# Optimization experiments

Hardware: AMD Instinct MI355X
Metric: run time of the kernel (lower is better)

Reference implementation:

```python
import jax, jax.numpy as jnp
import numpy as np

B, S, E = 8, 1024, 1024
H, HS = 16, 64  # num_heads, head_size; H*HS == E


def setup_inputs() -> dict:
    key = jax.random.key(0)
    ks = jax.random.split(key, 6)
    scale = 1.0 / np.sqrt(E)
    x = jax.random.normal(ks[0], (B, S, E), dtype=jnp.float32)
    # per-head projection weights stacked: [H, E, HS] (Linear(n_embd, head_size, bias=False))
    Wq = jax.random.normal(ks[1], (H, E, HS), dtype=jnp.float32) * scale
    Wk = jax.random.normal(ks[2], (H, E, HS), dtype=jnp.float32) * scale
    Wv = jax.random.normal(ks[3], (H, E, HS), dtype=jnp.float32) * scale
    # output projection Linear(n_embd, n_embd): torch weight [out, in] plus bias
    Wproj = jax.random.normal(ks[4], (E, E), dtype=jnp.float32) * scale
    bproj = jax.random.normal(ks[5], (E,), dtype=jnp.float32) * scale
    return {"x": x, "Wq": Wq, "Wk": Wk, "Wv": Wv, "Wproj": Wproj, "bproj": bproj}


def reference(x, Wq, Wk, Wv, Wproj, bproj):
    # q,k,v: [B, H, S, HS]
    q = jnp.einsum('bse,hed->bhsd', x, Wq)
    k = jnp.einsum('bse,hed->bhsd', x, Wk)
    v = jnp.einsum('bse,hed->bhsd', x, Wv)
    scores = jnp.einsum('bhsd,bhtd->bhst', q, k) * (HS ** -0.5)  # [B,H,S,S]
    causal = jnp.tril(jnp.ones((S, S), dtype=bool))
    scores = jnp.where(causal, scores, jnp.finfo(scores.dtype).min)
    attn = jax.nn.softmax(scores, axis=-1)
    out = jnp.einsum('bhst,bhtd->bhsd', attn, v)         # [B,H,S,HS]
    out = out.transpose(0, 2, 1, 3).reshape(B, S, H * HS)  # concat heads -> [B,S,E]
    return out @ Wproj.T + bproj  # dropout p=0 is identity
```

## Files before the change

kernel.cpp:

```cpp
#include <hip/hip_runtime.h>
#include <stdint.h>

#define DEVI __device__ __forceinline__

typedef __attribute__((ext_vector_type(8))) short bf16x8;
typedef __attribute__((ext_vector_type(4))) float floatx4;
typedef __attribute__((ext_vector_type(16))) float floatx16;

constexpr int Bb = 8, Ss = 1024, Ee = 1024, Hh = 16, HSs = 64;
constexpr int Mq = Bb * Ss;
constexpr int Nqkv = 3 * Hh * HSs;
constexpr int Kd = Ee;

DEVI unsigned short f2bf(float x) {
  union { float f; uint32_t u; } v; v.f = x;
  uint32_t r = v.u + 0x7FFFu + ((v.u >> 16) & 1u);
  return (unsigned short)(r >> 16);
}

DEVI uint32_t pk2(float a, float b) {
  return (uint32_t)f2bf(a) | ((uint32_t)f2bf(b) << 16);
}

DEVI bf16x8 mkfrag(uint32_t a, uint32_t b, uint32_t c, uint32_t d) {
  union { uint32_t u[4]; bf16x8 v; } x;
  x.u[0] = a; x.u[1] = b; x.u[2] = c; x.u[3] = d;
  return x.v;
}

DEVI floatx4 mfma16(bf16x8 a, bf16x8 b, floatx4 c) {
  return __builtin_amdgcn_mfma_f32_16x16x32_bf16(a, b, c, 0, 0, 0);
}
DEVI floatx16 mfma32(bf16x8 a, bf16x8 b, floatx16 c) {
  return __builtin_amdgcn_mfma_f32_32x32x16_bf16(a, b, c, 0, 0, 0);
}

DEVI void gload_lds16(const void* g, void* l) {
  __builtin_amdgcn_global_load_lds(
      (const __attribute__((address_space(1))) uint32_t*)(uintptr_t)g,
      (__attribute__((address_space(3))) uint32_t*)(uint32_t)(uintptr_t)l,
      16, 0, 0);
}

__global__ void cvt_f32_bf16(const float* __restrict__ in, unsigned short* __restrict__ out, int n) {
  int i = (blockIdx.x * blockDim.x + threadIdx.x) * 4;
  if (i >= n) return;
  float4 v = *(const float4*)&in[i];
  ushort4 o;
  o.x = f2bf(v.x); o.y = f2bf(v.y); o.z = f2bf(v.z); o.w = f2bf(v.w);
  *(ushort4*)(void*)&out[i] = o;
}

__global__ void cvt_wqkv(const float* __restrict__ Wq, const float* __restrict__ Wk,
                         const float* __restrict__ Wv, unsigned short* __restrict__ out) {
  __shared__ float tile[64][65];
  const int k0 = blockIdx.x * 64;
  const int hh = blockIdx.y;
  const int qkv = hh >> 4, h = hh & 15;
  const float* W = (qkv == 0) ? Wq : ((qkv == 1) ? Wk : Wv);
  const float scale = (qkv == 0) ? (0.125f * 1.44269504f) : 1.0f;
  const float* src = W + (size_t)h * Ee * HSs;
  const int c = threadIdx.x & 63, r4 = threadIdx.x >> 6;
#pragma unroll
  for (int rr = 0; rr < 16; ++rr) {
    int row = rr * 4 + r4;
    tile[row][c] = src[(size_t)(k0 + row) * HSs + c] * scale;
  }
  __syncthreads();
  const int base_n = qkv * 1024 + h * 64;
#pragma unroll
  for (int rr = 0; rr < 16; ++rr) {
    int hs = rr * 4 + r4;
    out[(size_t)(base_n + hs) * Kd + k0 + c] = f2bf(tile[c][hs]);
  }
}

__global__ __launch_bounds__(256, 4) void gemm_qkv_db32(
    const unsigned short* __restrict__ A, const unsigned short* __restrict__ Bt,
    unsigned short* __restrict__ Qb, unsigned short* __restrict__ Kb,
    unsigned short* __restrict__ Vtb, int Kdim) {
  __shared__ __align__(16) unsigned short As[2][128 * 32];
  __shared__ __align__(16) unsigned short Bs[2][128 * 32];
  const int tid = threadIdx.x;
  const int lane = tid & 63;
  const int wid = tid >> 6;
  const int wm = wid >> 1, wn = wid & 1;
  const int m0 = blockIdx.y * 128;
  const int n0 = blockIdx.x * 128;
  const int srow = lane >> 2;
  const int NT = Kdim >> 5;

  floatx4 acc[4][4];
#pragma unroll
  for (int i = 0; i < 4; ++i)
#pragma unroll
    for (int j = 0; j < 4; ++j) acc[i][j] = (floatx4)0.f;

  auto stage = [&](int kt, int b) {
#pragma unroll
    for (int i = 0; i < 2; ++i) {
      const int g = wid * 2 + i;
      const int row = g * 16 + srow;
      const int sch = (lane & 3) ^ ((row + (row >> 2)) & 3);
      gload_lds16(A + (size_t)(m0 + row) * Kdim + kt * 32 + sch * 8, &As[b][g * 512]);
      gload_lds16(Bt + (size_t)(n0 + row) * Kdim + kt * 32 + sch * 8, &Bs[b][g * 512]);
    }
  };

  stage(0, 0);
  __syncthreads();

  const int c = lane >> 4;
  for (int kt = 0; kt < NT; ++kt) {
    const int cur = kt & 1;
    if (kt + 1 < NT) stage(kt + 1, cur ^ 1);
    const unsigned short* Ap = As[cur];
    const unsigned short* Bp = Bs[cur];
    bf16x8 af[4], bf[4];
#pragma unroll
    for (int i = 0; i < 4; ++i) {
      const int ra = wm * 64 + i * 16 + (lane & 15);
      af[i] = *(const bf16x8*)&Ap[ra * 32 + ((c ^ ((ra + (ra >> 2)) & 3)) << 3)];
      const int rb = wn * 64 + i * 16 + (lane & 15);
      bf[i] = *(const bf16x8*)&Bp[rb * 32 + ((c ^ ((rb + (rb >> 2)) & 3)) << 3)];
    }
#pragma unroll
    for (int i = 0; i < 4; ++i)
#pragma unroll
      for (int j = 0; j < 4; ++j) acc[i][j] = mfma16(af[i], bf[j], acc[i][j]);
    __syncthreads();
  }

  const int mrow0 = m0 + wm * 64 + ((lane >> 4) << 2);
  const int ncol0 = n0 + wn * 64 + (lane & 15);
#pragma unroll
  for (int i = 0; i < 4; ++i) {
#pragma unroll
    for (int j = 0; j < 4; ++j) {
      const int n = ncol0 + j * 16;
      const int qkv = n >> 10;
      const int h = (n & 1023) >> 6;
      const int hs = n & 63;
#pragma unroll
      for (int r = 0; r < 4; ++r) {
        const int m = mrow0 + i * 16 + r;
        const int b = m >> 10, s = m & 1023;
        const unsigned short bv = f2bf(acc[i][j][r]);
        if (qkv == 0)
          Qb[(((size_t)b * Hh + h) * Ss + s) * HSs + hs] = bv;
        else if (qkv == 1)
          Kb[(((size_t)b * Hh + h) * Ss + s) * HSs + hs] = bv;
        else
          Vtb[(((size_t)b * Hh + h) * HSs + hs) * Ss + s] = bv;
      }
    }
  }
}

__global__ __launch_bounds__(256, 2) void gemm_proj(
    const unsigned short* __restrict__ A, const unsigned short* __restrict__ Bt,
    float* __restrict__ Out, const float* __restrict__ bias, int Ndim, int Kdim) {
  __shared__ __align__(16) unsigned short As[128 * 64];
  __shared__ __align__(16) unsigned short Bs[128 * 64];
  const int tid = threadIdx.x;
  const int lane = tid & 63;
  const int wid = tid >> 6;
  const int wm = wid >> 1, wn = wid & 1;
  const int m0 = blockIdx.y * 128;
  const int n0 = blockIdx.x * 128;

  floatx4 acc[4][4];
#pragma unroll
  for (int i = 0; i < 4; ++i)
#pragma unroll
    for (int j = 0; j < 4; ++j) acc[i][j] = (floatx4)0.f;

  const int srow = lane >> 3;
  const int schunk = (lane & 7) ^ srow;

  for (int kt = 0; kt < Kdim; kt += 64) {
#pragma unroll
    for (int j = 0; j < 4; ++j) {
      const int g = wid * 4 + j;
      const int row = g * 8 + srow;
      gload_lds16(A + (size_t)(m0 + row) * Kdim + kt + schunk * 8, &As[g * 8 * 64]);
      gload_lds16(Bt + (size_t)(n0 + row) * Kdim + kt + schunk * 8, &Bs[g * 8 * 64]);
    }
    __syncthreads();
#pragma unroll
    for (int kk = 0; kk < 2; ++kk) {
      const int c = kk * 4 + (lane >> 4);
      bf16x8 af[4], bf[4];
#pragma unroll
      for (int i = 0; i < 4; ++i) {
        const int ra = wm * 64 + i * 16 + (lane & 15);
        af[i] = *(const bf16x8*)&As[ra * 64 + ((c ^ (ra & 7)) << 3)];
        const int rb = wn * 64 + i * 16 + (lane & 15);
        bf[i] = *(const bf16x8*)&Bs[rb * 64 + ((c ^ (rb & 7)) << 3)];
      }
#pragma unroll
      for (int i = 0; i < 4; ++i)
#pragma unroll
        for (int j = 0; j < 4; ++j) acc[i][j] = mfma16(af[i], bf[j], acc[i][j]);
    }
    __syncthreads();
  }

  const int mrow0 = m0 + wm * 64 + ((lane >> 4) << 2);
  const int ncol0 = n0 + wn * 64 + (lane & 15);
#pragma unroll
  for (int j = 0; j < 4; ++j) {
    const int n = ncol0 + j * 16;
    const float bj = bias[n];
#pragma unroll
    for (int i = 0; i < 4; ++i) {
#pragma unroll
      for (int r = 0; r < 4; ++r) {
        const int m = mrow0 + i * 16 + r;
        Out[(size_t)m * Ndim + n] = acc[i][j][r] + bj;
      }
    }
  }
}

__global__ __launch_bounds__(512, 4) void attn(
    const unsigned short* __restrict__ Qb, const unsigned short* __restrict__ Kb,
    const unsigned short* __restrict__ Vtb, unsigned short* __restrict__ Ob) {
  __shared__ __align__(16) unsigned short Ks[3][64 * 64];
  __shared__ __align__(16) unsigned short Vs[3][64 * 64];

  const int tid = threadIdx.x;
  const int lane = tid & 63;
  const int wid = tid >> 6;
  const int ln = lane & 31;
  const int hi = lane >> 5;
  const int bh = blockIdx.x & 127;
  const int qs = blockIdx.x >> 7;
  const int q0 = (3 - qs) * 256;
  const int bI = bh >> 4, hI = bh & 15;
  const unsigned short* Qp = Qb + (size_t)bh * Ss * HSs;
  const unsigned short* Kp = Kb + (size_t)bh * Ss * HSs;
  const unsigned short* Vp = Vtb + (size_t)bh * HSs * Ss;
  const int qw = q0 + wid * 32;
  const int q = qw + ln;

  bf16x8 qf[4];
#pragma unroll
  for (int kc = 0; kc < 4; ++kc)
    qf[kc] = *(const bf16x8*)&Qp[(size_t)q * 64 + kc * 16 + hi * 8];

  floatx16 oacc[2];
  oacc[0] = (floatx16)0.f;
  oacc[1] = (floatx16)0.f;
  float mrow = -3.0e38f, lrow = 0.f;

  const int srow = lane >> 3;
  const int schunk = (lane & 7) ^ srow;
  const int nt = (q0 >> 6) + 4;

  auto stageKV = [&](int t, int b) {
    const int row = wid * 8 + srow;
    gload_lds16(Kp + (size_t)(t * 64 + row) * 64 + schunk * 8, &Ks[b][wid * 512]);
    gload_lds16(Vp + (size_t)row * Ss + t * 64 + schunk * 8, &Vs[b][wid * 512]);
  };

  stageKV(0, 0);
  stageKV(1, 1);
  asm volatile("s_waitcnt vmcnt(2)" ::: "memory");
  __builtin_amdgcn_s_barrier();

  for (int t = 0; t < nt; ++t) {
    const int cur = t % 3;
    const bool pf = (t + 2 < nt);
    if (pf) stageKV(t + 2, (t + 2) % 3);
    const int t0 = t * 64;

    if (t0 <= qw + 31) {
      const unsigned short* Kc = Ks[cur];
      const unsigned short* Vc = Vs[cur];
      floatx16 sc[2];
#pragma unroll
      for (int tt = 0; tt < 2; ++tt) {
        floatx16 s = (floatx16)0.f;
        __builtin_amdgcn_s_setprio(1);
#pragma unroll
        for (int kc = 0; kc < 4; ++kc) {
          const int row = tt * 32 + ln;
          bf16x8 kf = *(const bf16x8*)&Kc[row * 64 + ((((kc << 1) | hi) ^ (ln & 7)) << 3)];
          s = mfma32(kf, qf[kc], s);
        }
        __builtin_amdgcn_s_setprio(0);
        sc[tt] = s;
      }
      if (t0 + 63 > qw) {
#pragma unroll
        for (int tt = 0; tt < 2; ++tt)
#pragma unroll
          for (int r = 0; r < 16; ++r) {
            const int tg = t0 + tt * 32 + (r & 3) + 8 * (r >> 2) + 4 * hi;
            if (tg > q) sc[tt][r] = -1e30f;
          }
      }
      float mx = sc[0][0];
#pragma unroll
      for (int tt = 0; tt < 2; ++tt)
#pragma unroll
        for (int r = 0; r < 16; ++r) mx = fmaxf(mx, sc[tt][r]);
      mx = fmaxf(mx, __shfl_xor(mx, 32));
      const float mnew = fmaxf(mrow, mx);
      const float scal = __builtin_amdgcn_exp2f(mrow - mnew);
      mrow = mnew;
      float ss = 0.f;
#pragma unroll
      for (int tt = 0; tt < 2; ++tt)
#pragma unroll
        for (int r = 0; r < 16; ++r) {
          const float p = __builtin_amdgcn_exp2f(sc[tt][r] - mnew);
          sc[tt][r] = p;
          ss += p;
        }
      ss += __shfl_xor(ss, 32);
      lrow = lrow * scal + ss;
#pragma unroll
      for (int dt = 0; dt < 2; ++dt)
#pragma unroll
        for (int r = 0; r < 16; ++r) oacc[dt][r] *= scal;

      bf16x8 pf_[4];
#pragma unroll
      for (int tt = 0; tt < 2; ++tt)
#pragma unroll
        for (int fb = 0; fb < 2; ++fb) {
          const int b = fb * 8;
          const uint32_t w0 = pk2(sc[tt][b + 0], sc[tt][b + 1]);
          const uint32_t w1 = pk2(sc[tt][b + 2], sc[tt][b + 3]);
          const uint32_t w2 = pk2(sc[tt][b + 4], sc[tt][b + 5]);
          const uint32_t w3 = pk2(sc[tt][b + 6], sc[tt][b + 7]);
          const uint32_t x0 = (uint32_t)__shfl_xor((int)w0, 32);
          const uint32_t x1 = (uint32_t)__shfl_xor((int)w1, 32);
          const uint32_t x2 = (uint32_t)__shfl_xor((int)w2, 32);
          const uint32_t x3 = (uint32_t)__shfl_xor((int)w3, 32);
          pf_[tt * 2 + fb] = mkfrag(hi ? x2 : w0, hi ? x3 : w1, hi ? w2 : x0, hi ? w3 : x1);
        }
#pragma unroll
      for (int dt = 0; dt < 2; ++dt) {
        const int row = dt * 32 + ln;
        __builtin_amdgcn_s_setprio(1);
#pragma unroll
        for (int kc = 0; kc < 4; ++kc) {
          bf16x8 vf = *(const bf16x8*)&Vc[row * 64 + ((((kc << 1) | hi) ^ (ln & 7)) << 3)];
          oacc[dt] = mfma32(vf, pf_[kc], oacc[dt]);
        }
        __builtin_amdgcn_s_setprio(0);
      }
    }

    if (pf) { asm volatile("s_waitcnt vmcnt(2)" ::: "memory"); }
    else    { asm volatile("s_waitcnt vmcnt(0)" ::: "memory"); }
    __builtin_amdgcn_s_barrier();
  }

  const float inv = 1.0f / lrow;
  unsigned short* Op = Ob + ((size_t)bI * Ss + q) * Ee + hI * 64;
#pragma unroll
  for (int dt = 0; dt < 2; ++dt)
#pragma unroll
    for (int g4 = 0; g4 < 4; ++g4) {
      ushort4 o;
      o.x = f2bf(oacc[dt][g4 * 4 + 0] * inv);
      o.y = f2bf(oacc[dt][g4 * 4 + 1] * inv);
      o.z = f2bf(oacc[dt][g4 * 4 + 2] * inv);
      o.w = f2bf(oacc[dt][g4 * 4 + 3] * inv);
      *(ushort4*)(void*)&Op[dt * 32 + g4 * 8 + hi * 4] = o;
    }
}

extern "C" void kernel_launch(void* const* d_in, const int* in_sizes, int n_in,
                              void* d_out, int out_size, void* d_ws, size_t ws_size,
                              hipStream_t stream) {
  const float* x = (const float*)d_in[0];
  const float* Wq = (const float*)d_in[1];
  const float* Wk = (const float*)d_in[2];
  const float* Wv = (const float*)d_in[3];
  const float* Wproj = (const float*)d_in[4];
  const float* bproj = (const float*)d_in[5];
  float* out = (float*)d_out;

  char* ws = (char*)d_ws;
  unsigned short* xb     = (unsigned short*)(ws);
  unsigned short* wqkvb  = (unsigned short*)(ws + (16u << 20));
  unsigned short* wprojb = (unsigned short*)(ws + (22u << 20));
  unsigned short* Qb     = (unsigned short*)(ws + (24u << 20));
  unsigned short* Kb     = (unsigned short*)(ws + (40u << 20));
  unsigned short* Vtb    = (unsigned short*)(ws + (56u << 20));
  unsigned short* Obuf   = (unsigned short*)(ws + (72u << 20));

  cvt_f32_bf16<<<8192, 256, 0, stream>>>(x, xb, Bb * Ss * Ee);
  cvt_wqkv<<<dim3(16, 48), 256, 0, stream>>>(Wq, Wk, Wv, wqkvb);
  cvt_f32_bf16<<<1024, 256, 0, stream>>>(Wproj, wprojb, Ee * Ee);
  gemm_qkv_db32<<<dim3(Nqkv / 128, Mq / 128), 256, 0, stream>>>(
      xb, wqkvb, Qb, Kb, Vtb, Kd);
  attn<<<512, 512, 0, stream>>>(Qb, Kb, Vtb, Obuf);
  gemm_proj<<<dim3(Ee / 128, Mq / 128), 256, 0, stream>>>(
      Obuf, wprojb, out, bproj, Ee, Kd);
}
```

Before: 170.2 us.

## Retile QKV GEMM to 128x256 blocks with K=64 steps and vectorized V^T stores

The QKV projection GEMM moves from 256-thread 128x128 double-buffered K=32 tiles to 512-thread 128x256 single-buffered K=64 tiles with an XOR swizzle on 8 chunks. The wider tile raises operand reuse per LDS load and halves the number of K iterations and barriers. The V-transpose epilogue now writes four consecutive sequence positions as one ushort4 store instead of scattered 2-byte writes. Dropping double buffering exposes global-load latency inside each iteration, which may offset the gains.

New measurement: 384.8 us. +126.1%, slower.

```diff
diff --git a/kernel.cpp b/kernel.cpp
--- a/kernel.cpp
+++ b/kernel.cpp
@@ -75,20 +75,21 @@
   }
 }
 
-__global__ __launch_bounds__(256, 4) void gemm_qkv_db32(
+__global__ __launch_bounds__(512, 6) void gemm_qkv(
     const unsigned short* __restrict__ A, const unsigned short* __restrict__ Bt,
     unsigned short* __restrict__ Qb, unsigned short* __restrict__ Kb,
     unsigned short* __restrict__ Vtb, int Kdim) {
-  __shared__ __align__(16) unsigned short As[2][128 * 32];
-  __shared__ __align__(16) unsigned short Bs[2][128 * 32];
+  __shared__ __align__(16) unsigned short As[128 * 64];
+  __shared__ __align__(16) unsigned short Bs[256 * 64];
   const int tid = threadIdx.x;
   const int lane = tid & 63;
   const int wid = tid >> 6;
-  const int wm = wid >> 1, wn = wid & 1;
+  const int wm = wid >> 2, wn = wid & 3;
   const int m0 = blockIdx.y * 128;
-  const int n0 = blockIdx.x * 128;
-  const int srow = lane >> 2;
-  const int NT = Kdim >> 5;
+  const int n0 = blockIdx.x * 256;
+  const int srow = lane >> 3;
+  const int schunk = (lane & 7) ^ srow;
+  const int NT = Kdim >> 6;
 
   floatx4 acc[4][4];
 #pragma unroll
@@ -96,62 +97,75 @@
 #pragma unroll
     for (int j = 0; j < 4; ++j) acc[i][j] = (floatx4)0.f;
 
-  auto stage = [&](int kt, int b) {
+  for (int kt = 0; kt < NT; ++kt) {
 #pragma unroll
     for (int i = 0; i < 2; ++i) {
-      const int g = wid * 2 + i;
-      const int row = g * 16 + srow;
-      const int sch = (lane & 3) ^ ((row + (row >> 2)) & 3);
-      gload_lds16(A + (size_t)(m0 + row) * Kdim + kt * 32 + sch * 8, &As[b][g * 512]);
-      gload_lds16(Bt + (size_t)(n0 + row) * Kdim + kt * 32 + sch * 8, &Bs[b][g * 512]);
-    }
-  };
-
-  stage(0, 0);
-  __syncthreads();
-
-  const int c = lane >> 4;
-  for (int kt = 0; kt < NT; ++kt) {
-    const int cur = kt & 1;
-    if (kt + 1 < NT) stage(kt + 1, cur ^ 1);
-    const unsigned short* Ap = As[cur];
-    const unsigned short* Bp = Bs[cur];
-    bf16x8 af[4], bf[4];
+      const int g = wid + i * 8;
+      const int row = g * 8 + srow;
+      gload_lds16(A + (size_t)(m0 + row) * Kdim + kt * 64 + schunk * 8, &As[g * 512]);
+    }
 #pragma unroll
     for (int i = 0; i < 4; ++i) {
-      const int ra = wm * 64 + i * 16 + (lane & 15);
-      af[i] = *(const bf16x8*)&Ap[ra * 32 + ((c ^ ((ra + (ra >> 2)) & 3)) << 3)];
-      const int rb = wn * 64 + i * 16 + (lane & 15);
-      bf[i] = *(const bf16x8*)&Bp[rb * 32 + ((c ^ ((rb + (rb >> 2)) & 3)) << 3)];
-    }
-#pragma unroll
-    for (int i = 0; i < 4; ++i)
-#pragma unroll
-      for (int j = 0; j < 4; ++j) acc[i][j] = mfma16(af[i], bf[j], acc[i][j]);
+      const int g = wid + i * 8;
+      const int row = g * 8 + srow;
+      gload_lds16(Bt + (size_t)(n0 + row) * Kdim + kt * 64 + schunk * 8, &Bs[g * 512]);
+    }
+    __syncthreads();
+#pragma unroll
+    for (int kk = 0; kk < 2; ++kk) {
+      const int c = kk * 4 + (lane >> 4);
+      bf16x8 af[4], bf[4];
+#pragma unroll
+      for (int i = 0; i < 4; ++i) {
+        const int ra = wm * 64 + i * 16 + (lane & 15);
+        af[i] = *(const bf16x8*)&As[ra * 64 + ((c ^ (ra & 7)) << 3)];
+        const int rb = wn * 64 + i * 16 + (lane & 15);
+        bf[i] = *(const bf16x8*)&Bs[rb * 64 + ((c ^ (rb & 7)) << 3)];
+      }
+#pragma unroll
+      for (int i = 0; i < 4; ++i)
+#pragma unroll
+        for (int j = 0; j < 4; ++j) acc[i][j] = mfma16(af[i], bf[j], acc[i][j]);
+    }
     __syncthreads();
   }
 
   const int mrow0 = m0 + wm * 64 + ((lane >> 4) << 2);
   const int ncol0 = n0 + wn * 64 + (lane & 15);
-#pragma unroll
-  for (int i = 0; i < 4; ++i) {
-#pragma unroll
-    for (int j = 0; j < 4; ++j) {
-      const int n = ncol0 + j * 16;
-      const int qkv = n >> 10;
-      const int h = (n & 1023) >> 6;
-      const int hs = n & 63;
-#pragma unroll
-      for (int r = 0; r < 4; ++r) {
-        const int m = mrow0 + i * 16 + r;
-        const int b = m >> 10, s = m & 1023;
-        const unsigned short bv = f2bf(acc[i][j][r]);
-        if (qkv == 0)
-          Qb[(((size_t)b * Hh + h) * Ss + s) * HSs + hs] = bv;
-        else if (qkv == 1)
-          Kb[(((size_t)b * Hh + h) * Ss + s) * HSs + hs] = bv;
-        else
-          Vtb[(((size_t)b * Hh + h) * HSs + hs) * Ss + s] = bv;
+  const int qkv = n0 >> 10;
+  if (qkv == 2) {
+#pragma unroll
+    for (int i = 0; i < 4; ++i) {
+      const int m = mrow0 + i * 16;
+      const int b = m >> 10, s = m & 1023;
+#pragma unroll
+      for (int j = 0; j < 4; ++j) {
+        const int n = ncol0 + j * 16;
+        const int h = (n & 1023) >> 6;
+        const int hs = n & 63;
+        ushort4 o;
+        o.x = f2bf(acc[i][j][0]);
+        o.y = f2bf(acc[i][j][1]);
+        o.z = f2bf(acc[i][j][2]);
+        o.w = f2bf(acc[i][j][3]);
+        *(ushort4*)(void*)&Vtb[(((size_t)b * Hh + h) * HSs + hs) * Ss + s] = o;
+      }
+    }
+  } else {
+    unsigned short* P = (qkv == 0) ? Qb : Kb;
+#pragma unroll
+    for (int i = 0; i < 4; ++i) {
+#pragma unroll
+      for (int j = 0; j < 4; ++j) {
+        const int n = ncol0 + j * 16;
+        const int h = (n & 1023) >> 6;
+        const int hs = n & 63;
+#pragma unroll
+        for (int r = 0; r < 4; ++r) {
+          const int m = mrow0 + i * 16 + r;
+          const int b = m >> 10, s = m & 1023;
+          P[(((size_t)b * Hh + h) * Ss + s) * HSs + hs] = f2bf(acc[i][j][r]);
+        }
       }
     }
   }
@@ -398,7 +412,7 @@
   cvt_f32_bf16<<<8192, 256, 0, stream>>>(x, xb, Bb * Ss * Ee);
   cvt_wqkv<<<dim3(16, 48), 256, 0, stream>>>(Wq, Wk, Wv, wqkvb);
   cvt_f32_bf16<<<1024, 256, 0, stream>>>(Wproj, wprojb, Ee * Ee);
-  gemm_qkv_db32<<<dim3(Nqkv / 128, Mq / 128), 256, 0, stream>>>(
+  gemm_qkv<<<dim3(Nqkv / 256, Mq / 128), 512, 0, stream>>>(
       xb, wqkvb, Qb, Kb, Vtb, Kd);
   attn<<<512, 512, 0, stream>>>(Qb, Kb, Vtb, Obuf);
   gemm_proj<<<dim3(Ee / 128, Mq / 128), 256, 0, stream>>>(
```

## Replace double-buffered BK=32 QKV GEMM with single-buffered BK=64 tiles

Applied to the files above, without the earlier changes.

The QKV projection GEMM drops its double-buffered 32-wide K staging and instead loads a single 64-wide K tile per iteration, with an XOR swizzle over 8 chunks, then syncs and computes. Global-to-LDS loads no longer overlap with MFMA inside a block; latency hiding now relies on other resident blocks. Launch bounds drop from 4 to 2 blocks per SM, which relaxes register pressure but also lowers occupancy. This looks like a revert toward a simpler single-buffer kernel with fewer barriers per K step.

Result: faster. 158.1 us (-7.1%).

```diff
diff --git a/kernel.cpp b/kernel.cpp
--- a/kernel.cpp
+++ b/kernel.cpp
@@ -75,20 +75,18 @@
   }
 }
 
-__global__ __launch_bounds__(256, 4) void gemm_qkv_db32(
+__global__ __launch_bounds__(256, 2) void gemm_qkv(
     const unsigned short* __restrict__ A, const unsigned short* __restrict__ Bt,
     unsigned short* __restrict__ Qb, unsigned short* __restrict__ Kb,
     unsigned short* __restrict__ Vtb, int Kdim) {
-  __shared__ __align__(16) unsigned short As[2][128 * 32];
-  __shared__ __align__(16) unsigned short Bs[2][128 * 32];
+  __shared__ __align__(16) unsigned short As[128 * 64];
+  __shared__ __align__(16) unsigned short Bs[128 * 64];
   const int tid = threadIdx.x;
   const int lane = tid & 63;
   const int wid = tid >> 6;
   const int wm = wid >> 1, wn = wid & 1;
   const int m0 = blockIdx.y * 128;
   const int n0 = blockIdx.x * 128;
-  const int srow = lane >> 2;
-  const int NT = Kdim >> 5;
 
   floatx4 acc[4][4];
 #pragma unroll
@@ -96,38 +94,34 @@
 #pragma unroll
     for (int j = 0; j < 4; ++j) acc[i][j] = (floatx4)0.f;
 
-  auto stage = [&](int kt, int b) {
-#pragma unroll
-    for (int i = 0; i < 2; ++i) {
-      const int g = wid * 2 + i;
-      const int row = g * 16 + srow;
-      const int sch = (lane & 3) ^ ((row + (row >> 2)) & 3);
-      gload_lds16(A + (size_t)(m0 + row) * Kdim + kt * 32 + sch * 8, &As[b][g * 512]);
-      gload_lds16(Bt + (size_t)(n0 + row) * Kdim + kt * 32 + sch * 8, &Bs[b][g * 512]);
-    }
-  };
-
-  stage(0, 0);
-  __syncthreads();
-
-  const int c = lane >> 4;
-  for (int kt = 0; kt < NT; ++kt) {
-    const int cur = kt & 1;
-    if (kt + 1 < NT) stage(kt + 1, cur ^ 1);
-    const unsigned short* Ap = As[cur];
-    const unsigned short* Bp = Bs[cur];
-    bf16x8 af[4], bf[4];
-#pragma unroll
-    for (int i = 0; i < 4; ++i) {
-      const int ra = wm * 64 + i * 16 + (lane & 15);
-      af[i] = *(const bf16x8*)&Ap[ra * 32 + ((c ^ ((ra + (ra >> 2)) & 3)) << 3)];
-      const int rb = wn * 64 + i * 16 + (lane & 15);
-      bf[i] = *(const bf16x8*)&Bp[rb * 32 + ((c ^ ((rb + (rb >> 2)) & 3)) << 3)];
-    }
-#pragma unroll
-    for (int i = 0; i < 4; ++i)
-#pragma unroll
-      for (int j = 0; j < 4; ++j) acc[i][j] = mfma16(af[i], bf[j], acc[i][j]);
+  const int srow = lane >> 3;
+  const int schunk = (lane & 7) ^ srow;
+
+  for (int kt = 0; kt < Kdim; kt += 64) {
+#pragma unroll
+    for (int j = 0; j < 4; ++j) {
+      const int g = wid * 4 + j;
+      const int row = g * 8 + srow;
+      gload_lds16(A + (size_t)(m0 + row) * Kdim + kt + schunk * 8, &As[g * 8 * 64]);
+      gload_lds16(Bt + (size_t)(n0 + row) * Kdim + kt + schunk * 8, &Bs[g * 8 * 64]);
+    }
+    __syncthreads();
+#pragma unroll
+    for (int kk = 0; kk < 2; ++kk) {
+      const int c = kk * 4 + (lane >> 4);
+      bf16x8 af[4], bf[4];
+#pragma unroll
+      for (int i = 0; i < 4; ++i) {
+        const int ra = wm * 64 + i * 16 + (lane & 15);
+        af[i] = *(const bf16x8*)&As[ra * 64 + ((c ^ (ra & 7)) << 3)];
+        const int rb = wn * 64 + i * 16 + (lane & 15);
+        bf[i] = *(const bf16x8*)&Bs[rb * 64 + ((c ^ (rb & 7)) << 3)];
+      }
+#pragma unroll
+      for (int i = 0; i < 4; ++i)
+#pragma unroll
+        for (int j = 0; j < 4; ++j) acc[i][j] = mfma16(af[i], bf[j], acc[i][j]);
+    }
     __syncthreads();
   }
 
@@ -398,7 +392,7 @@
   cvt_f32_bf16<<<8192, 256, 0, stream>>>(x, xb, Bb * Ss * Ee);
   cvt_wqkv<<<dim3(16, 48), 256, 0, stream>>>(Wq, Wk, Wv, wqkvb);
   cvt_f32_bf16<<<1024, 256, 0, stream>>>(Wproj, wprojb, Ee * Ee);
-  gemm_qkv_db32<<<dim3(Nqkv / 128, Mq / 128), 256, 0, stream>>>(
+  gemm_qkv<<<dim3(Nqkv / 128, Mq / 128), 256, 0, stream>>>(
       xb, wqkvb, Qb, Kb, Vtb, Kd);
   attn<<<512, 512, 0, stream>>>(Qb, Kb, Vtb, Obuf);
   gemm_proj<<<dim3(Ee / 128, Mq / 128), 256, 0, stream>>>(
```
